# Optimization experiments

Measured on AMD Instinct MI355X. Metric: run time of the kernel, lower is better.

The kernel has to match this reference:

```python
import jax, jax.numpy as jnp
import numpy as np

B, S, D, H = 4, 2048, 768, 4
DH = D // H  # 192


def setup_inputs() -> dict:
    key = jax.random.key(0)
    ks = jax.random.split(key, 5)
    std = 1.0 / np.sqrt(D)
    return {
        "x": jax.random.normal(ks[0], (B, S, D), dtype=jnp.float32),
        "Wq": jax.random.normal(ks[1], (D, D), dtype=jnp.float32) * std,
        "Wk": jax.random.normal(ks[2], (D, D), dtype=jnp.float32) * std,
        "Wv": jax.random.normal(ks[3], (D, D), dtype=jnp.float32) * std,
        "Wo": jax.random.normal(ks[4], (D, D), dtype=jnp.float32) * std,
    }


def reference(x, Wq, Wk, Wv, Wo):
    b, s, d = x.shape
    # nn.Linear(bias=False): y = x @ W.T
    q = (x @ Wq.T).reshape(b, s, H, DH).transpose(0, 2, 1, 3)  # [B,H,S,DH]
    k = (x @ Wk.T).reshape(b, s, H, DH).transpose(0, 2, 1, 3)
    v = (x @ Wv.T).reshape(b, s, H, DH).transpose(0, 2, 1, 3)
    scale = jnp.sqrt(jnp.asarray(DH, dtype=q.dtype))
    logits = jnp.einsum("bhqd,bhkd->bhqk", q, k) / scale  # [B,H,S,S]
    causal = jnp.tril(jnp.ones((s, s), dtype=bool))
    logits = jnp.where(causal, logits, -jnp.inf)
    A = jax.nn.softmax(logits, axis=-1)
    preout = jnp.einsum("bhqk,bhkd->bhqd", A, v)  # [B,H,S,DH]
    # W_O = rearrange(Wo.T, '(h dh) dm -> h dh dm'); sum over heads == full Wo
    W_O = Wo.T.reshape(H, DH, D)
    out = jnp.einsum("bhsd,hdm->bsm", preout, W_O)  # [B,S,D]
    return out
```

## Files before the change

### kernel.cpp

```cpp
#include <hip/hip_runtime.h>
#include <hip/hip_bf16.h>

constexpr int CB = 4, CS = 2048, CD = 768, CH = 4, CDH = 192;
constexpr int CM = CB * CS;

typedef float f32x4 __attribute__((ext_vector_type(4)));
typedef float fx4 __attribute__((ext_vector_type(4)));
typedef __bf16 bx8 __attribute__((ext_vector_type(8)));
typedef unsigned short u16;
typedef u16 u16x8 __attribute__((ext_vector_type(8)));
typedef u16 u16x4 __attribute__((ext_vector_type(4)));

static __device__ __forceinline__ u16 f32_bf16(float f) {
  unsigned u = __builtin_bit_cast(unsigned, f);
  u += 0x7FFFu + ((u >> 16) & 1u);
  return (u16)(u >> 16);
}

static __device__ __forceinline__ f32x4 mfma16(bx8 a, bx8 b, f32x4 c) {
  return __builtin_amdgcn_mfma_f32_16x16x32_bf16(a, b, c, 0, 0, 0);
}

__global__ void __launch_bounds__(256) convert_all(
    const float* __restrict__ x, const float* __restrict__ wq,
    const float* __restrict__ wk, const float* __restrict__ wv,
    const float* __restrict__ wo, u16* __restrict__ xb, u16* __restrict__ wqb,
    u16* __restrict__ wkb, u16* __restrict__ wvb, u16* __restrict__ wob) {
  const float* srcs[5] = {x, wq, wk, wv, wo};
  u16* dsts[5] = {xb, wqb, wkb, wvb, wob};
  const int n4s[5] = {CM * CD / 4, CD * CD / 4, CD * CD / 4, CD * CD / 4,
                      CD * CD / 4};
  const int gsz = gridDim.x * blockDim.x;
  const int gid = blockIdx.x * blockDim.x + threadIdx.x;
#pragma unroll
  for (int sg = 0; sg < 5; ++sg) {
    const fx4* src = (const fx4*)srcs[sg];
    u16* dst = dsts[sg];
    const int n4 = n4s[sg];
    for (int i = gid; i < n4; i += gsz) {
      fx4 v = src[i];
      u16x4 o;
      o[0] = f32_bf16(v[0]);
      o[1] = f32_bf16(v[1]);
      o[2] = f32_bf16(v[2]);
      o[3] = f32_bf16(v[3]);
      *(u16x4*)&dst[(size_t)i * 4] = o;
    }
  }
}

template <bool OUT_BF16>
__global__ void __launch_bounds__(256) gemm_bt(
    const u16* __restrict__ A, const u16* __restrict__ Bw0,
    const u16* __restrict__ Bw1, const u16* __restrict__ Bw2,
    void* __restrict__ C0, void* __restrict__ C1, void* __restrict__ C2,
    int M, int N, int K) {
  constexpr int LDK = 72;
  __shared__ u16 As[128][LDK];
  __shared__ u16 Bs[128][LDK];
  const int z = blockIdx.z;
  const u16* Bw = (z == 0) ? Bw0 : ((z == 1) ? Bw1 : Bw2);
  void* Cv = (z == 0) ? C0 : ((z == 1) ? C1 : C2);
  const int m0 = blockIdx.x * 128;
  const int n0 = blockIdx.y * 128;
  const int tid = threadIdx.x;
  const int wave = tid >> 6, lane = tid & 63;
  const int wr = wave >> 1, wc = wave & 1;
  const int lr = lane & 15, lhi = lane >> 4;

  f32x4 acc[4][4];
  const f32x4 zero = {0.f, 0.f, 0.f, 0.f};
#pragma unroll
  for (int i = 0; i < 4; ++i)
#pragma unroll
    for (int j = 0; j < 4; ++j) acc[i][j] = zero;

  for (int kk = 0; kk < K; kk += 64) {
#pragma unroll
    for (int r = 0; r < 4; ++r) {
      const int id = tid + r * 256;
      const int row = id >> 3, ch = id & 7;
      *(u16x8*)&As[row][ch * 8] =
          *(const u16x8*)&A[(size_t)(m0 + row) * K + kk + ch * 8];
      *(u16x8*)&Bs[row][ch * 8] =
          *(const u16x8*)&Bw[(size_t)(n0 + row) * K + kk + ch * 8];
    }
    __syncthreads();
#pragma unroll
    for (int ks = 0; ks < 2; ++ks) {
      bx8 af[4], bf[4];
#pragma unroll
      for (int mf = 0; mf < 4; ++mf)
        af[mf] = *(const bx8*)&As[wr * 64 + mf * 16 + lr][ks * 32 + lhi * 8];
#pragma unroll
      for (int nf = 0; nf < 4; ++nf)
        bf[nf] = *(const bx8*)&Bs[wc * 64 + nf * 16 + lr][ks * 32 + lhi * 8];
#pragma unroll
      for (int mf = 0; mf < 4; ++mf)
#pragma unroll
        for (int nf = 0; nf < 4; ++nf)
          acc[mf][nf] = mfma16(af[mf], bf[nf], acc[mf][nf]);
    }
    __syncthreads();
  }
#pragma unroll
  for (int mf = 0; mf < 4; ++mf)
#pragma unroll
    for (int nf = 0; nf < 4; ++nf)
#pragma unroll
      for (int r = 0; r < 4; ++r) {
        const int row = m0 + wr * 64 + mf * 16 + lhi * 4 + r;
        const int col = n0 + wc * 64 + nf * 16 + lr;
        if constexpr (OUT_BF16)
          ((u16*)Cv)[(size_t)row * N + col] = f32_bf16(acc[mf][nf][r]);
        else
          ((float*)Cv)[(size_t)row * N + col] = acc[mf][nf][r];
      }
}

__global__ void __launch_bounds__(256, 2) flash_attn(
    const u16* __restrict__ Qg, const u16* __restrict__ Kg,
    const u16* __restrict__ Vg, u16* __restrict__ Og) {
  __shared__ u16 Ks[12288];
  __shared__ u16 Vs[12288];
  __shared__ u16 Ps[4][16][72];
  const int g = blockIdx.x;
  const int qt = (g < 256) ? (g >> 4) : (31 - ((g - 256) >> 4));
  const int bh = g & 15;
  const int b = bh >> 2, h = bh & 3;
  const int tid = threadIdx.x;
  const int wave = tid >> 6, lane = tid & 63;
  const int lr = lane & 15, lhi = lane >> 4;
  const size_t base_elem = ((size_t)b * CS) * CD + (size_t)h * CDH;
  constexpr float scale = 0.07216878364870323f;
  const f32x4 zero = {0.f, 0.f, 0.f, 0.f};

  int kOff[6], vOff[6];
#pragma unroll
  for (int r = 0; r < 6; ++r) {
    const int p = tid + r * 256;
    {
      const int k = p / 24, c16 = p - k * 24;
      const unsigned swz = ((unsigned)(c16 * 16)) ^ ((unsigned)((k & 7) << 4));
      kOff[r] = k * CD + (int)(swz >> 1);
    }
    {
      const int blk = p >> 3, kq = (p >> 1) & 3, dh = p & 1;
      const int kk = ((blk & 15) << 2) + kq;
      const int d = ((blk >> 4) << 4) + dh * 8;
      vOff[r] = kk * CD + d;
    }
  }
  const unsigned vlds0 =
      (unsigned)(unsigned long long)(__attribute__((address_space(3)))
                                         u16*)&Vs[0];

  float m_run = -INFINITY, l_run = 0.f;
  f32x4 acc[12];
#pragma unroll
  for (int nf = 0; nf < 12; ++nf) acc[nf] = zero;

  bx8 qf[6];
  {
    const size_t qoff = base_elem + (size_t)(qt * 64 + wave * 16 + lr) * CD;
#pragma unroll
    for (int c = 0; c < 6; ++c)
      qf[c] = *(const bx8*)&Qg[qoff + c * 32 + lhi * 8];
  }

  u16x8 kreg[6], vreg[6];
  auto ldregs = [&](int kt) {
    const u16* kg = Kg + base_elem + (size_t)(kt * 64) * CD;
    const u16* vg = Vg + base_elem + (size_t)(kt * 64) * CD;
#pragma unroll
    for (int r = 0; r < 6; ++r) {
      kreg[r] = *(const u16x8*)&kg[kOff[r]];
      vreg[r] = *(const u16x8*)&vg[vOff[r]];
    }
  };

  ldregs(0);
  const int qg = qt * 64 + wave * 16 + lr;

  for (int i = 0; i <= qt; ++i) {
    __syncthreads();
#pragma unroll
    for (int r = 0; r < 6; ++r) {
      *(u16x8*)&Ks[(size_t)(tid + r * 256) * 8] = kreg[r];
      *(u16x8*)&Vs[(size_t)(tid + r * 256) * 8] = vreg[r];
    }
    if (i < qt) ldregs(i + 1);
    __syncthreads();

    const int k0 = i * 64;
    const bool diag = (i == qt);
    f32x4 st[4];
#pragma unroll
    for (int mf = 0; mf < 4; ++mf) st[mf] = zero;
#pragma unroll
    for (int c = 0; c < 6; ++c)
#pragma unroll
      for (int mf = 0; mf < 4; ++mf) {
        const int row = mf * 16 + lr;
        const unsigned off =
            ((unsigned)(c * 64 + lhi * 16)) ^ ((unsigned)((row & 7) << 4));
        const bx8 kf =
            *(const bx8*)((const char*)Ks + (size_t)row * 384 + off);
        st[mf] = mfma16(kf, qf[c], st[mf]);
      }
    float pvv[16];
#pragma unroll
    for (int mf = 0; mf < 4; ++mf)
#pragma unroll
      for (int r = 0; r < 4; ++r) {
        float s = st[mf][r] * scale;
        if (diag && (k0 + mf * 16 + lhi * 4 + r > qg)) s = -INFINITY;
        pvv[mf * 4 + r] = s;
      }
    float mx = pvv[0];
#pragma unroll
    for (int t = 1; t < 16; ++t) mx = fmaxf(mx, pvv[t]);
    mx = fmaxf(mx, __shfl_xor(mx, 16, 64));
    mx = fmaxf(mx, __shfl_xor(mx, 32, 64));
    const bool skip = __all(mx - m_run <= 8.0f);
    if (!skip) {
      const float mnew = fmaxf(m_run, mx);
      const float alpha = __expf(m_run - mnew);
      float afr[4];
#pragma unroll
      for (int r = 0; r < 4; ++r) afr[r] = __shfl(alpha, lhi * 4 + r, 64);
#pragma unroll
      for (int nf = 0; nf < 12; ++nf)
#pragma unroll
        for (int r = 0; r < 4; ++r) acc[nf][r] *= afr[r];
      l_run *= alpha;
      m_run = mnew;
    }
    float rs = 0.f;
#pragma unroll
    for (int t = 0; t < 16; ++t) {
      const float e = __expf(pvv[t] - m_run);
      pvv[t] = e;
      rs += e;
    }
    rs += __shfl_xor(rs, 16, 64);
    rs += __shfl_xor(rs, 32, 64);
    l_run += rs;
#pragma unroll
    for (int mf = 0; mf < 4; ++mf)
#pragma unroll
      for (int rp = 0; rp < 2; ++rp) {
        const unsigned w0 = f32_bf16(pvv[mf * 4 + rp * 2]);
        const unsigned w1 = f32_bf16(pvv[mf * 4 + rp * 2 + 1]);
        *(unsigned*)&Ps[wave][lr][mf * 16 + lhi * 4 + rp * 2] =
            w0 | (w1 << 16);
      }
    const bx8 pf0 = *(const bx8*)&Ps[wave][lr][lhi * 8];
    const bx8 pf1 = *(const bx8*)&Ps[wave][lr][32 + lhi * 8];
#pragma unroll
    for (int gg = 0; gg < 3; ++gg) {
      u16x4 tl[4][2], th[4][2];
#pragma unroll
      for (int q4 = 0; q4 < 4; ++q4)
#pragma unroll
        for (int c2 = 0; c2 < 2; ++c2) {
          const int nf = gg * 4 + q4;
          const unsigned va =
              vlds0 + (unsigned)((nf * 16 + c2 * 8 + lhi * 2) * 128 + lr * 8);
          asm volatile("ds_read_b64_tr_b16 %0, %2\n\t"
                       "ds_read_b64_tr_b16 %1, %2 offset:128"
                       : "=&v"(tl[q4][c2]), "=&v"(th[q4][c2])
                       : "v"(va));
        }
      asm volatile("s_waitcnt lgkmcnt(0)" ::: "memory");
      __builtin_amdgcn_sched_barrier(0);
#pragma unroll
      for (int q4 = 0; q4 < 4; ++q4)
#pragma unroll
        for (int c2 = 0; c2 < 2; ++c2) {
          const int nf = gg * 4 + q4;
          const u16x8 vv = __builtin_shufflevector(tl[q4][c2], th[q4][c2], 0,
                                                   1, 2, 3, 4, 5, 6, 7);
          acc[nf] = mfma16(c2 == 0 ? pf0 : pf1, __builtin_bit_cast(bx8, vv),
                           acc[nf]);
        }
    }
  }

#pragma unroll
  for (int r = 0; r < 4; ++r) {
    const float lb = __shfl(l_run, lhi * 4 + r, 64);
    const float linv = 1.0f / lb;
    const size_t orow =
        base_elem + (size_t)(qt * 64 + wave * 16 + lhi * 4 + r) * CD;
#pragma unroll
    for (int nf = 0; nf < 12; ++nf)
      Og[orow + nf * 16 + lr] = f32_bf16(acc[nf][r] * linv);
  }
}

extern "C" void kernel_launch(void* const* d_in, const int* in_sizes, int n_in,
                              void* d_out, int out_size, void* d_ws,
                              size_t ws_size, hipStream_t stream) {
  (void)in_sizes;
  (void)n_in;
  (void)out_size;
  (void)ws_size;
  const float* x = (const float*)d_in[0];
  const float* wq = (const float*)d_in[1];
  const float* wk = (const float*)d_in[2];
  const float* wv = (const float*)d_in[3];
  const float* wo = (const float*)d_in[4];
  float* out = (float*)d_out;
  char* ws = (char*)d_ws;
  const size_t big = (size_t)CM * CD * 2;
  const size_t wsz = (size_t)CD * CD * 2;
  u16* xb = (u16*)ws;
  u16* qb = (u16*)(ws + big);
  u16* kb = (u16*)(ws + 2 * big);
  u16* vb = (u16*)(ws + 3 * big);
  u16* wqb = (u16*)(ws + 4 * big);
  u16* wkb = (u16*)(ws + 4 * big + wsz);
  u16* wvb = (u16*)(ws + 4 * big + 2 * wsz);
  u16* wob = (u16*)(ws + 4 * big + 3 * wsz);
  u16* pob = xb;

  convert_all<<<dim3(1024), dim3(256), 0, stream>>>(x, wq, wk, wv, wo, xb, wqb,
                                                    wkb, wvb, wob);
  gemm_bt<true><<<dim3(64, 6, 3), dim3(256), 0, stream>>>(
      xb, wqb, wkb, wvb, (void*)qb, (void*)kb, (void*)vb, CM, CD, CD);
  flash_attn<<<dim3(512), dim3(256), 0, stream>>>(qb, kb, vb, pob);
  gemm_bt<false><<<dim3(64, 6, 1), dim3(256), 0, stream>>>(
      pob, wob, wob, wob, (void*)out, (void*)out, (void*)out, CM, CD, CD);
}
```

Measured before the change: 158.9 us.

## Split flash attention across KV ranges with combine pass, register prefetch in GEMM

Flash attention now processes 128-row query tiles, two 16-row groups per wave, and splits long causal rows into KV-range chunks scheduled by a static table. Partial outputs and their max/sum statistics go to scratch in the output buffer, and a new combine kernel merges them. K/V tiles are loaded straight into LDS with global_load_lds instead of through registers. The GEMM gains register double-buffering and s_setprio around its MFMA blocks, and convert_all gets a larger grid. The aim is to balance causal work across blocks and reuse each K/V tile for more queries, at the cost of an extra kernel launch and scratch traffic.

```diff
diff --git a/kernel.cpp b/kernel.cpp
--- a/kernel.cpp
+++ b/kernel.cpp
@@ -16,9 +16,18 @@
   u += 0x7FFFu + ((u >> 16) & 1u);
   return (u16)(u >> 16);
 }
+static __device__ __forceinline__ float bf16_f32(u16 v) {
+  return __builtin_bit_cast(float, (unsigned)v << 16);
+}
 
 static __device__ __forceinline__ f32x4 mfma16(bx8 a, bx8 b, f32x4 c) {
   return __builtin_amdgcn_mfma_f32_16x16x32_bf16(a, b, c, 0, 0, 0);
+}
+
+static __device__ __forceinline__ void load_lds16(const u16* g, u16* l) {
+  __builtin_amdgcn_global_load_lds(
+      (const __attribute__((address_space(1))) unsigned int*)g,
+      (__attribute__((address_space(3))) unsigned int*)l, 16, 0, 0);
 }
 
 __global__ void __launch_bounds__(256) convert_all(
@@ -75,16 +84,28 @@
 #pragma unroll
     for (int j = 0; j < 4; ++j) acc[i][j] = zero;
 
-  for (int kk = 0; kk < K; kk += 64) {
+  u16x8 areg[4], breg[4];
+  auto ldregs = [&](int kk) {
 #pragma unroll
     for (int r = 0; r < 4; ++r) {
       const int id = tid + r * 256;
       const int row = id >> 3, ch = id & 7;
-      *(u16x8*)&As[row][ch * 8] =
-          *(const u16x8*)&A[(size_t)(m0 + row) * K + kk + ch * 8];
-      *(u16x8*)&Bs[row][ch * 8] =
-          *(const u16x8*)&Bw[(size_t)(n0 + row) * K + kk + ch * 8];
-    }
+      areg[r] = *(const u16x8*)&A[(size_t)(m0 + row) * K + kk + ch * 8];
+      breg[r] = *(const u16x8*)&Bw[(size_t)(n0 + row) * K + kk + ch * 8];
+    }
+  };
+
+  ldregs(0);
+  for (int kk = 0; kk < K; kk += 64) {
+    __syncthreads();
+#pragma unroll
+    for (int r = 0; r < 4; ++r) {
+      const int id = tid + r * 256;
+      const int row = id >> 3, ch = id & 7;
+      *(u16x8*)&As[row][ch * 8] = areg[r];
+      *(u16x8*)&Bs[row][ch * 8] = breg[r];
+    }
+    if (kk + 64 < K) ldregs(kk + 64);
     __syncthreads();
 #pragma unroll
     for (int ks = 0; ks < 2; ++ks) {
@@ -95,13 +116,14 @@
 #pragma unroll
       for (int nf = 0; nf < 4; ++nf)
         bf[nf] = *(const bx8*)&Bs[wc * 64 + nf * 16 + lr][ks * 32 + lhi * 8];
+      __builtin_amdgcn_s_setprio(1);
 #pragma unroll
       for (int mf = 0; mf < 4; ++mf)
 #pragma unroll
         for (int nf = 0; nf < 4; ++nf)
           acc[mf][nf] = mfma16(af[mf], bf[nf], acc[mf][nf]);
-    }
-    __syncthreads();
+      __builtin_amdgcn_s_setprio(0);
+    }
   }
 #pragma unroll
   for (int mf = 0; mf < 4; ++mf)
@@ -118,15 +140,39 @@
       }
 }
 
+#define PKE(q, k0, k1, p)                                               \
+  ((unsigned)(q) | ((unsigned)(k0) << 4) | ((unsigned)(k1) << 9) |      \
+   ((unsigned)((p) + 1) << 15))
+__device__ const unsigned FA_TBL[32] = {
+    PKE(10, 0, 11, 0),   PKE(10, 11, 22, 1),  PKE(15, 0, 11, 2),
+    PKE(15, 11, 22, 3),  PKE(4, 0, 10, -1),   PKE(9, 0, 10, 4),
+    PKE(9, 10, 20, 5),   PKE(13, 0, 10, 6),   PKE(14, 0, 10, 7),
+    PKE(14, 10, 20, 8),  PKE(14, 20, 30, 9),  PKE(15, 22, 32, 10),
+    PKE(8, 0, 9, 11),    PKE(8, 9, 18, 12),   PKE(12, 0, 9, 13),
+    PKE(12, 9, 18, 14),  PKE(0, 0, 2, -1),    PKE(1, 0, 4, -1),
+    PKE(2, 0, 6, -1),    PKE(5, 0, 6, 15),    PKE(5, 6, 12, 16),
+    PKE(6, 0, 7, 17),    PKE(6, 7, 14, 18),   PKE(3, 0, 8, -1),
+    PKE(7, 0, 8, 19),    PKE(7, 8, 16, 20),   PKE(11, 0, 8, 21),
+    PKE(11, 8, 16, 22),  PKE(11, 16, 24, 23), PKE(12, 18, 26, 24),
+    PKE(13, 10, 19, 25), PKE(13, 19, 28, 26)};
+
 __global__ void __launch_bounds__(256, 2) flash_attn(
     const u16* __restrict__ Qg, const u16* __restrict__ Kg,
-    const u16* __restrict__ Vg, u16* __restrict__ Og) {
+    const u16* __restrict__ Vg, u16* __restrict__ Og, u16* __restrict__ pO,
+    float* __restrict__ pML) {
   __shared__ u16 Ks[12288];
   __shared__ u16 Vs[12288];
-  __shared__ u16 Ps[4][16][72];
-  const int g = blockIdx.x;
-  const int qt = (g < 256) ? (g >> 4) : (31 - ((g - 256) >> 4));
-  const int bh = g & 15;
+  __shared__ u16 Ps[4][32][72];
+  const int i0_ = blockIdx.x;
+  const int xcd = i0_ & 7;
+  const int r_ = i0_ >> 3;
+  const int bh = xcd * 2 + (r_ & 1);
+  const int s = r_ >> 1;
+  const unsigned e = FA_TBL[s];
+  const int q128 = (int)(e & 15u);
+  const int kt0 = (int)((e >> 4) & 31u);
+  const int kt1 = (int)((e >> 9) & 63u);
+  const int pidx = (int)((e >> 15) & 63u) - 1;
   const int b = bh >> 2, h = bh & 3;
   const int tid = threadIdx.x;
   const int wave = tid >> 6, lane = tid & 63;
@@ -155,48 +201,48 @@
       (unsigned)(unsigned long long)(__attribute__((address_space(3)))
                                          u16*)&Vs[0];
 
-  float m_run = -INFINITY, l_run = 0.f;
-  f32x4 acc[12];
-#pragma unroll
-  for (int nf = 0; nf < 12; ++nf) acc[nf] = zero;
-
-  bx8 qf[6];
+  float m_run[2] = {-INFINITY, -INFINITY};
+  float l_run[2] = {0.f, 0.f};
+  f32x4 acc[2][12];
+#pragma unroll
+  for (int qg = 0; qg < 2; ++qg)
+#pragma unroll
+    for (int nf = 0; nf < 12; ++nf) acc[qg][nf] = zero;
+
+  bx8 qf[2][6];
   {
-    const size_t qoff = base_elem + (size_t)(qt * 64 + wave * 16 + lr) * CD;
-#pragma unroll
-    for (int c = 0; c < 6; ++c)
-      qf[c] = *(const bx8*)&Qg[qoff + c * 32 + lhi * 8];
-  }
-
-  u16x8 kreg[6], vreg[6];
-  auto ldregs = [&](int kt) {
-    const u16* kg = Kg + base_elem + (size_t)(kt * 64) * CD;
-    const u16* vg = Vg + base_elem + (size_t)(kt * 64) * CD;
-#pragma unroll
-    for (int r = 0; r < 6; ++r) {
-      kreg[r] = *(const u16x8*)&kg[kOff[r]];
-      vreg[r] = *(const u16x8*)&vg[vOff[r]];
-    }
-  };
-
-  ldregs(0);
-  const int qg = qt * 64 + wave * 16 + lr;
-
-  for (int i = 0; i <= qt; ++i) {
+    const int qrow0 = q128 * 128 + wave * 32;
+#pragma unroll
+    for (int qg = 0; qg < 2; ++qg) {
+      const size_t qoff = base_elem + (size_t)(qrow0 + qg * 16 + lr) * CD;
+#pragma unroll
+      for (int c = 0; c < 6; ++c)
+        qf[qg][c] = *(const bx8*)&Qg[qoff + c * 32 + lhi * 8];
+    }
+  }
+
+  for (int kt = kt0; kt < kt1; ++kt) {
     __syncthreads();
-#pragma unroll
-    for (int r = 0; r < 6; ++r) {
-      *(u16x8*)&Ks[(size_t)(tid + r * 256) * 8] = kreg[r];
-      *(u16x8*)&Vs[(size_t)(tid + r * 256) * 8] = vreg[r];
-    }
-    if (i < qt) ldregs(i + 1);
+    {
+      const u16* kg = Kg + base_elem + (size_t)(kt * 64) * CD;
+      const u16* vg = Vg + base_elem + (size_t)(kt * 64) * CD;
+#pragma unroll
+      for (int r = 0; r < 6; ++r)
+        load_lds16(kg + kOff[r], &Ks[(size_t)(tid + r * 256) * 8]);
+#pragma unroll
+      for (int r = 0; r < 6; ++r)
+        load_lds16(vg + vOff[r], &Vs[(size_t)(tid + r * 256) * 8]);
+    }
     __syncthreads();
 
-    const int k0 = i * 64;
-    const bool diag = (i == qt);
-    f32x4 st[4];
-#pragma unroll
-    for (int mf = 0; mf < 4; ++mf) st[mf] = zero;
+    const int k0 = kt * 64;
+    const bool diag = (kt >= 2 * q128);
+    f32x4 st[2][4];
+#pragma unroll
+    for (int qg = 0; qg < 2; ++qg)
+#pragma unroll
+      for (int mf = 0; mf < 4; ++mf) st[qg][mf] = zero;
+    __builtin_amdgcn_s_setprio(1);
 #pragma unroll
     for (int c = 0; c < 6; ++c)
 #pragma unroll
@@ -206,57 +252,69 @@
             ((unsigned)(c * 64 + lhi * 16)) ^ ((unsigned)((row & 7) << 4));
         const bx8 kf =
             *(const bx8*)((const char*)Ks + (size_t)row * 384 + off);
-        st[mf] = mfma16(kf, qf[c], st[mf]);
-      }
-    float pvv[16];
-#pragma unroll
-    for (int mf = 0; mf < 4; ++mf)
-#pragma unroll
-      for (int r = 0; r < 4; ++r) {
-        float s = st[mf][r] * scale;
-        if (diag && (k0 + mf * 16 + lhi * 4 + r > qg)) s = -INFINITY;
-        pvv[mf * 4 + r] = s;
-      }
-    float mx = pvv[0];
-#pragma unroll
-    for (int t = 1; t < 16; ++t) mx = fmaxf(mx, pvv[t]);
-    mx = fmaxf(mx, __shfl_xor(mx, 16, 64));
-    mx = fmaxf(mx, __shfl_xor(mx, 32, 64));
-    const bool skip = __all(mx - m_run <= 8.0f);
-    if (!skip) {
-      const float mnew = fmaxf(m_run, mx);
-      const float alpha = __expf(m_run - mnew);
-      float afr[4];
-#pragma unroll
-      for (int r = 0; r < 4; ++r) afr[r] = __shfl(alpha, lhi * 4 + r, 64);
-#pragma unroll
-      for (int nf = 0; nf < 12; ++nf)
-#pragma unroll
-        for (int r = 0; r < 4; ++r) acc[nf][r] *= afr[r];
-      l_run *= alpha;
-      m_run = mnew;
-    }
-    float rs = 0.f;
-#pragma unroll
-    for (int t = 0; t < 16; ++t) {
-      const float e = __expf(pvv[t] - m_run);
-      pvv[t] = e;
-      rs += e;
-    }
-    rs += __shfl_xor(rs, 16, 64);
-    rs += __shfl_xor(rs, 32, 64);
-    l_run += rs;
-#pragma unroll
-    for (int mf = 0; mf < 4; ++mf)
-#pragma unroll
-      for (int rp = 0; rp < 2; ++rp) {
-        const unsigned w0 = f32_bf16(pvv[mf * 4 + rp * 2]);
-        const unsigned w1 = f32_bf16(pvv[mf * 4 + rp * 2 + 1]);
-        *(unsigned*)&Ps[wave][lr][mf * 16 + lhi * 4 + rp * 2] =
-            w0 | (w1 << 16);
-      }
-    const bx8 pf0 = *(const bx8*)&Ps[wave][lr][lhi * 8];
-    const bx8 pf1 = *(const bx8*)&Ps[wave][lr][32 + lhi * 8];
+        st[0][mf] = mfma16(kf, qf[0][c], st[0][mf]);
+        st[1][mf] = mfma16(kf, qf[1][c], st[1][mf]);
+      }
+    __builtin_amdgcn_s_setprio(0);
+
+#pragma unroll
+    for (int qg = 0; qg < 2; ++qg) {
+      const int qg_row = q128 * 128 + wave * 32 + qg * 16 + lr;
+      float pvv[16];
+#pragma unroll
+      for (int mf = 0; mf < 4; ++mf)
+#pragma unroll
+        for (int r = 0; r < 4; ++r) {
+          float sv = st[qg][mf][r] * scale;
+          if (diag && (k0 + mf * 16 + lhi * 4 + r > qg_row)) sv = -INFINITY;
+          pvv[mf * 4 + r] = sv;
+        }
+      float mx = pvv[0];
+#pragma unroll
+      for (int tt = 1; tt < 16; ++tt) mx = fmaxf(mx, pvv[tt]);
+      mx = fmaxf(mx, __shfl_xor(mx, 16, 64));
+      mx = fmaxf(mx, __shfl_xor(mx, 32, 64));
+      const bool skip = __all(mx - m_run[qg] <= 8.0f);
+      if (!skip) {
+        const float mnew = fmaxf(m_run[qg], mx);
+        const float alpha = __expf(m_run[qg] - mnew);
+        float afr[4];
+#pragma unroll
+        for (int r = 0; r < 4; ++r)
+          afr[r] = __shfl(alpha, lhi * 4 + r, 64);
+#pragma unroll
+        for (int nf = 0; nf < 12; ++nf)
+#pragma unroll
+          for (int r = 0; r < 4; ++r) acc[qg][nf][r] *= afr[r];
+        l_run[qg] *= alpha;
+        m_run[qg] = mnew;
+      }
+      float rs = 0.f;
+#pragma unroll
+      for (int tt = 0; tt < 16; ++tt) {
+        const float ev = __expf(pvv[tt] - m_run[qg]);
+        pvv[tt] = ev;
+        rs += ev;
+      }
+      rs += __shfl_xor(rs, 16, 64);
+      rs += __shfl_xor(rs, 32, 64);
+      l_run[qg] += rs;
+#pragma unroll
+      for (int mf = 0; mf < 4; ++mf)
+#pragma unroll
+        for (int rp = 0; rp < 2; ++rp) {
+          const unsigned w0 = f32_bf16(pvv[mf * 4 + rp * 2]);
+          const unsigned w1 = f32_bf16(pvv[mf * 4 + rp * 2 + 1]);
+          *(unsigned*)&Ps[wave][qg * 16 + lr][mf * 16 + lhi * 4 + rp * 2] =
+              w0 | (w1 << 16);
+        }
+    }
+
+    const bx8 pf[2][2] = {
+        {*(const bx8*)&Ps[wave][lr][lhi * 8],
+         *(const bx8*)&Ps[wave][lr][32 + lhi * 8]},
+        {*(const bx8*)&Ps[wave][16 + lr][lhi * 8],
+         *(const bx8*)&Ps[wave][16 + lr][32 + lhi * 8]}};
 #pragma unroll
     for (int gg = 0; gg < 3; ++gg) {
       u16x4 tl[4][2], th[4][2];
@@ -274,6 +332,7 @@
         }
       asm volatile("s_waitcnt lgkmcnt(0)" ::: "memory");
       __builtin_amdgcn_sched_barrier(0);
+      __builtin_amdgcn_s_setprio(1);
 #pragma unroll
       for (int q4 = 0; q4 < 4; ++q4)
 #pragma unroll
@@ -281,21 +340,108 @@
           const int nf = gg * 4 + q4;
           const u16x8 vv = __builtin_shufflevector(tl[q4][c2], th[q4][c2], 0,
                                                    1, 2, 3, 4, 5, 6, 7);
-          acc[nf] = mfma16(c2 == 0 ? pf0 : pf1, __builtin_bit_cast(bx8, vv),
-                           acc[nf]);
+          const bx8 vb = __builtin_bit_cast(bx8, vv);
+          acc[0][nf] = mfma16(pf[0][c2], vb, acc[0][nf]);
+          acc[1][nf] = mfma16(pf[1][c2], vb, acc[1][nf]);
         }
-    }
-  }
-
-#pragma unroll
-  for (int r = 0; r < 4; ++r) {
-    const float lb = __shfl(l_run, lhi * 4 + r, 64);
-    const float linv = 1.0f / lb;
-    const size_t orow =
-        base_elem + (size_t)(qt * 64 + wave * 16 + lhi * 4 + r) * CD;
-#pragma unroll
-    for (int nf = 0; nf < 12; ++nf)
-      Og[orow + nf * 16 + lr] = f32_bf16(acc[nf][r] * linv);
+      __builtin_amdgcn_s_setprio(0);
+    }
+  }
+
+  if (pidx < 0) {
+#pragma unroll
+    for (int qg = 0; qg < 2; ++qg)
+#pragma unroll
+      for (int r = 0; r < 4; ++r) {
+        const float lb = __shfl(l_run[qg], lhi * 4 + r, 64);
+        const float linv = 1.0f / lb;
+        const size_t orow =
+            base_elem +
+            (size_t)(q128 * 128 + wave * 32 + qg * 16 + lhi * 4 + r) * CD;
+#pragma unroll
+        for (int nf = 0; nf < 12; ++nf)
+          Og[orow + nf * 16 + lr] = f32_bf16(acc[qg][nf][r] * linv);
+      }
+  } else {
+    const int pbase = bh * 27 + pidx;
+    if (lhi == 0) {
+#pragma unroll
+      for (int qg = 0; qg < 2; ++qg) {
+        pML[pbase * 256 + wave * 32 + qg * 16 + lr] = m_run[qg];
+        pML[pbase * 256 + 128 + wave * 32 + qg * 16 + lr] = l_run[qg];
+      }
+    }
+#pragma unroll
+    for (int qg = 0; qg < 2; ++qg)
+#pragma unroll
+      for (int r = 0; r < 4; ++r) {
+        const float lb = __shfl(l_run[qg], lhi * 4 + r, 64);
+        const float linv = 1.0f / lb;
+        u16* dst = pO + ((size_t)pbase * 128 + wave * 32 + qg * 16 +
+                         lhi * 4 + r) *
+                            192;
+#pragma unroll
+        for (int nf = 0; nf < 12; ++nf)
+          dst[nf * 16 + lr] = f32_bf16(acc[qg][nf][r] * linv);
+      }
+  }
+}
+
+#define CBE(n, p0, p1, p2) \
+  ((unsigned)(n) | ((unsigned)(p0) << 2) | ((unsigned)(p1) << 8) | \
+   ((unsigned)(p2) << 14))
+__device__ const unsigned CB_TBL[11] = {
+    CBE(2, 15, 16, 0), CBE(2, 17, 18, 0), CBE(2, 19, 20, 0),
+    CBE(2, 11, 12, 0), CBE(2, 4, 5, 0),   CBE(2, 0, 1, 0),
+    CBE(3, 21, 22, 23), CBE(3, 13, 14, 24), CBE(3, 6, 25, 26),
+    CBE(3, 7, 8, 9),    CBE(3, 2, 3, 10)};
+
+__global__ void __launch_bounds__(256) combine_qt(
+    const u16* __restrict__ pO, const float* __restrict__ pML,
+    u16* __restrict__ Og) {
+  const int cb = blockIdx.x;
+  const int bh = cb / 11, qi = cb % 11;
+  const int q128 = qi + 5;
+  const unsigned e = CB_TBL[qi];
+  const int n = (int)(e & 3u);
+  const int pid0 = (int)((e >> 2) & 63u);
+  const int pid1 = (int)((e >> 8) & 63u);
+  const int pid2 = (int)((e >> 14) & 63u);
+  const int b = bh >> 2, h = bh & 3;
+  const int tid = threadIdx.x;
+  const int row = tid >> 1, half = tid & 1;
+  float m[3], l[3];
+  const int pids[3] = {pid0, pid1, pid2};
+  for (int i = 0; i < n; ++i) {
+    m[i] = pML[(bh * 27 + pids[i]) * 256 + row];
+    l[i] = pML[(bh * 27 + pids[i]) * 256 + 128 + row];
+  }
+  float M = m[0];
+  for (int i = 1; i < n; ++i) M = fmaxf(M, m[i]);
+  float w[3], wsum = 0.f;
+  for (int i = 0; i < n; ++i) {
+    w[i] = l[i] * __expf(m[i] - M);
+    wsum += w[i];
+  }
+  const float inv = 1.0f / wsum;
+  const size_t obase =
+      ((size_t)b * CS + (size_t)q128 * 128 + row) * CD + h * CDH + half * 96;
+#pragma unroll
+  for (int c = 0; c < 12; ++c) {
+    float a8[8] = {0.f, 0.f, 0.f, 0.f, 0.f, 0.f, 0.f, 0.f};
+    for (int i = 0; i < n; ++i) {
+      const u16x8 v = *(const u16x8*)&pO[((size_t)(bh * 27 + pids[i]) * 128 +
+                                          row) *
+                                             192 +
+                                         half * 96 + c * 8];
+      const float f = w[i] * inv;
+#pragma unroll
+      for (int j = 0; j < 8; ++j) a8[j] += f * bf16_f32(v[j]);
+    }
+    u16x8 o;
+#pragma unroll
+    for (int j = 0; j < 8; ++j) o[j] = f32_bf16(a8[j]);
+    *(u16x8*)&Og[obase + c * 8] = o;
   }
 }
 
@@ -324,12 +470,15 @@
   u16* wvb = (u16*)(ws + 4 * big + 2 * wsz);
   u16* wob = (u16*)(ws + 4 * big + 3 * wsz);
   u16* pob = xb;
-
-  convert_all<<<dim3(1024), dim3(256), 0, stream>>>(x, wq, wk, wv, wo, xb, wqb,
+  u16* pO = (u16*)d_out;
+  float* pML = (float*)((char*)d_out + (size_t)16 * 27 * 128 * 192 * 2);
+
+  convert_all<<<dim3(2048), dim3(256), 0, stream>>>(x, wq, wk, wv, wo, xb, wqb,
                                                     wkb, wvb, wob);
   gemm_bt<true><<<dim3(64, 6, 3), dim3(256), 0, stream>>>(
       xb, wqb, wkb, wvb, (void*)qb, (void*)kb, (void*)vb, CM, CD, CD);
-  flash_attn<<<dim3(512), dim3(256), 0, stream>>>(qb, kb, vb, pob);
+  flash_attn<<<dim3(512), dim3(256), 0, stream>>>(qb, kb, vb, pob, pO, pML);
+  combine_qt<<<dim3(176), dim3(256), 0, stream>>>(pO, pML, pob);
   gemm_bt<false><<<dim3(64, 6, 1), dim3(256), 0, stream>>>(
       pob, wob, wob, wob, (void*)out, (void*)out, (void*)out, CM, CD, CD);
 }
```

New measurement: 153.0 us. -3.7%, faster.
